# Kernel optimization log

Hardware: AMD Instinct MI355X
Metric: run time of the kernel (lower is better)

## Reference

```python
import jax, jax.numpy as jnp
import numpy as np

B, H, C, R, S, NS = 32, 128, 512, 64, 4096, 8
D = C + R
T = B * S
MAX_POS = 8192


def setup_inputs() -> dict:
    key = jax.random.key(0)
    k0, k1, k2, k3, k4 = jax.random.split(key, 5)
    q = jax.random.normal(k0, (B, H, D), dtype=jnp.float32)
    k_buffer = jax.random.normal(k1, (T, 1, D), dtype=jnp.float32)
    v_buffer = jax.random.normal(k2, (T, 1, C), dtype=jnp.float32)
    cos_sin_cache = jax.random.normal(k3, (MAX_POS, R), dtype=jnp.float32)
    positions = jax.random.randint(k4, (B,), 0, MAX_POS, dtype=jnp.int64) if jax.config.jax_enable_x64 else jax.random.randint(k4, (B,), 0, MAX_POS, dtype=jnp.int32)
    kv_indptr = (jnp.arange(B + 1, dtype=jnp.int32) * S)
    kv_indices = jnp.arange(T, dtype=jnp.int32)
    return {
        "q": q, "k_buffer": k_buffer, "v_buffer": v_buffer,
        "cos_sin_cache": cos_sin_cache, "positions": positions,
        "kv_indptr": kv_indptr, "kv_indices": kv_indices,
        "num_kv_splits": 8, "kv_lora_rank": 512, "rotary_dim": 64,
        "use_rope": 1,
    }


def _rotate_half(x, half):
    return jnp.concatenate([-x[..., half:], x[..., :half]], axis=-1)


def reference(q, k_buffer, v_buffer, cos_sin_cache, positions, kv_indptr,
              kv_indices, num_kv_splits, kv_lora_rank, rotary_dim, use_rope):
    b, h, head_dim = q.shape
    c = kv_lora_rank
    r = k_buffer.shape[-1] - c  # qk_rope_head_dim
    sm_scale = 1.0 / (head_dim ** 0.5)
    half = rotary_dim // 2

    kb = k_buffer[:, 0, :]
    vb = v_buffer[:, 0, :]
    s = kv_indices.shape[0] // b  # uniform seq_len layout (kv_indptr = arange*S)
    idx = kv_indices.reshape(b, s)
    seq_len = kv_indptr[1:] - kv_indptr[:-1]  # [b]

    k_rows = kb[idx]            # [b, s, c+r]
    kv_c = k_rows[:, :, :c]     # [b, s, c]
    k_pe = k_rows[:, :, c:]     # [b, s, r]
    v = vb[idx]                 # [b, s, c]

    q_c = q[:, :, :c]           # [b, h, c]
    q_pe = q[:, :, c:]          # [b, h, r]

    if use_rope:
        cos = cos_sin_cache[positions, :half]            # [b, half]
        sin = cos_sin_cache[positions, half:rotary_dim]  # [b, half]
        cos2 = jnp.concatenate([cos, cos], axis=-1)      # [b, r] (r == rotary_dim)
        sin2 = jnp.concatenate([sin, sin], axis=-1)
        q_pe = q_pe * cos2[:, None, :] + _rotate_half(q_pe, half) * sin2[:, None, :]
        # only the last cached token gets RoPE applied to its k_pe
        last_kpe = k_pe[jnp.arange(b), seq_len - 1]      # [b, r]
        last_roped = last_kpe * cos2 + _rotate_half(last_kpe, half) * sin2
        is_last = jnp.arange(s)[None, :] == (seq_len - 1)[:, None]  # [b, s]
        k_pe = jnp.where(is_last[:, :, None], last_roped[:, None, :], k_pe)
        k_pe_tokens_out = last_roped.astype(q.dtype)
    else:
        k_pe_tokens_out = jnp.zeros((1,), dtype=q.dtype)

    scores = (jnp.einsum('bhc,bsc->bhs', q_c, kv_c)
              + jnp.einsum('bhr,bsr->bhs', q_pe, k_pe)) * sm_scale  # [b, h, s]

    pos_n = jnp.arange(s)
    klps = (seq_len + num_kv_splits - 1) // num_kv_splits   # kv_len_per_split, [b]
    split_id = pos_n[None, :] // klps[:, None]              # [b, s]
    valid = pos_n[None, :] < seq_len[:, None]

    neg_inf = jnp.float32(-jnp.inf)
    outs = []
    for sp in range(num_kv_splits):  # small, static loop over KV splits
        m = (split_id == sp) & valid                        # [b, s]
        sc = jnp.where(m[:, None, :], scores, neg_inf)
        mx = jnp.max(sc, axis=-1)                           # [b, h]
        p = jnp.exp(sc - mx[..., None])
        e_sum = jnp.sum(p, axis=-1)                         # [b, h]
        o = jnp.einsum('bhs,bsc->bhc', p, v) / e_sum[..., None]
        lse = mx + jnp.log(e_sum)                           # [b, h]
        outs.append(jnp.concatenate([o, lse[..., None]], axis=-1))
    att_out = jnp.stack(outs, axis=2).astype(jnp.float32)   # [b, h, NS, c+1]
    return att_out, k_pe_tokens_out
```

## Files before the change

### kernel.cpp

```cpp
#include <hip/hip_runtime.h>
#include <math.h>

#define B_    32
#define H_    128
#define C_    512
#define R_    64
#define S_    4096
#define NS_   8
#define D_    576
#define HALF_ 32
#define HT    32
#define KB    32
#define PK    584
#define PS    36
#define PP    40

typedef _Float16 half8   __attribute__((ext_vector_type(8)));
typedef _Float16 half4_t __attribute__((ext_vector_type(4)));
typedef float    f32x4   __attribute__((ext_vector_type(4)));


__global__ __launch_bounds__(256)
void rope_q_kernel(float* __restrict__ q, const float* __restrict__ cache,
                   const int* __restrict__ positions) {
    int t = blockIdx.x * 256 + threadIdx.x;
    if (t >= B_ * H_ * HALF_) return;
    int i = t & (HALF_ - 1);
    int h = (t >> 5) & (H_ - 1);
    int b = t >> 12;
    int pos = positions[b];
    float c = cache[pos * R_ + i];
    float s = cache[pos * R_ + HALF_ + i];
    float* qp = q + (size_t)(b * H_ + h) * D_ + C_;
    float lo = qp[i], hi = qp[i + HALF_];
    qp[i]         = lo * c - hi * s;
    qp[i + HALF_] = hi * c + lo * s;
}

__global__ __launch_bounds__(256)
void rope_k_kernel(float* __restrict__ kbuf, const float* __restrict__ cache,
                   const int* __restrict__ positions, const int* __restrict__ indptr,
                   const int* __restrict__ indices, float* __restrict__ out_tail) {
    int t = blockIdx.x * 256 + threadIdx.x;
    if (t >= B_ * HALF_) return;
    int i = t & (HALF_ - 1);
    int b = t >> 5;
    int seq = indptr[b + 1] - indptr[b];
    int row = indices[b * S_ + seq - 1];
    int pos = positions[b];
    float c = cache[pos * R_ + i];
    float s = cache[pos * R_ + HALF_ + i];
    float* kp = kbuf + (size_t)row * D_ + C_;
    float lo = kp[i], hi = kp[i + HALF_];
    float nlo = lo * c - hi * s;
    float nhi = hi * c + lo * s;
    kp[i] = nlo; kp[i + HALF_] = nhi;
    out_tail[b * R_ + i]         = nlo;
    out_tail[b * R_ + HALF_ + i] = nhi;
}

__global__ void zero_tail_kernel(float* p) { if (threadIdx.x == 0) p[0] = 0.f; }


__global__ __launch_bounds__(256, 2)
void mla_attn_kernel(const float* __restrict__ q, const float* __restrict__ kbuf,
                     const float* __restrict__ vbuf, const int* __restrict__ indptr,
                     const int* __restrict__ indices, float* __restrict__ out) {
    __shared__ _Float16 k_lds[KB * PK];
    __shared__ float    s_lds[HT * PS];
    __shared__ _Float16 p_lds[HT * PP];
    __shared__ int      rows_s[KB];
    __shared__ float    m_s[HT], l_s[HT], a_s[HT];

    const int blk   = blockIdx.x;
    const int xcd   = blk & 7;
    const int inner = blk >> 3;
    const int htile = inner & 3;
    const int bs    = ((inner >> 2) << 3) | xcd;
    const int b     = bs >> 3;
    const int sp    = bs & 7;
    const int h0    = htile * HT;

    const int t    = threadIdx.x;
    const int lane = t & 63;
    const int w    = t >> 6;
    const int hm   = w >> 1;
    const int hv   = w & 1;
    const int lr   = lane & 15;
    const int kg   = lane >> 4;

    const int seq   = indptr[b + 1] - indptr[b];
    const int klps  = (seq + NS_ - 1) / NS_;
    const int start = sp * klps;
    const int end   = min(start + klps, seq);

    half8 qf[18];
    {
        const float* qrow = q + (size_t)(b * H_ + h0 + hm * 16 + lr) * D_ + kg * 8;
        #pragma unroll
        for (int s = 0; s < 18; ++s) {
            f32x4 x0 = *(const f32x4*)(qrow + s * 32);
            f32x4 x1 = *(const f32x4*)(qrow + s * 32 + 4);
            half8 h;
            h[0] = (_Float16)x0[0]; h[1] = (_Float16)x0[1];
            h[2] = (_Float16)x0[2]; h[3] = (_Float16)x0[3];
            h[4] = (_Float16)x1[0]; h[5] = (_Float16)x1[1];
            h[6] = (_Float16)x1[2]; h[7] = (_Float16)x1[3];
            qf[s] = h;
        }
    }
    if (t < HT) { m_s[t] = -INFINITY; l_s[t] = 0.f; }

    f32x4 oacc[16];
    #pragma unroll
    for (int n = 0; n < 16; ++n) oacc[n] = (f32x4){0.f, 0.f, 0.f, 0.f};

    const float sm_scale = 1.0f / sqrtf((float)D_);
    const int nchunk = (end - start + KB - 1) / KB;

    for (int ch = 0; ch < nchunk; ++ch) {
        const int j0 = start + ch * KB;
        __syncthreads();

        {
            const int row = t >> 3;
            const int seg = t & 7;
            const int pos = min(j0 + row, end - 1);
            const int r   = indices[b * S_ + pos];
            if (seg == 0) rows_s[row] = r;
            const float* src = kbuf + (size_t)r * D_;
            _Float16* dst = k_lds + row * PK;
            #pragma unroll
            for (int i = 0; i < 18; ++i) {
                const int f = (seg + 8 * i) * 4;
                f32x4 x = *(const f32x4*)(src + f);
                half4_t hh;
                hh[0] = (_Float16)x[0]; hh[1] = (_Float16)x[1];
                hh[2] = (_Float16)x[2]; hh[3] = (_Float16)x[3];
                *(half4_t*)(dst + f) = hh;
            }
        }
        __syncthreads();

        {
            f32x4 sacc = (f32x4){0.f, 0.f, 0.f, 0.f};
            const _Float16* kp = k_lds + (hv * 16 + lr) * PK + kg * 8;
            #pragma unroll
            for (int s = 0; s < 18; ++s) {
                half8 bf = *(const half8*)(kp + s * 32);
                sacc = __builtin_amdgcn_mfma_f32_16x16x32_f16(qf[s], bf, sacc, 0, 0, 0);
            }
            #pragma unroll
            for (int r = 0; r < 4; ++r)
                s_lds[(hm * 16 + kg * 4 + r) * PS + hv * 16 + lr] = sacc[r] * sm_scale;
        }
        __syncthreads();

        {
            const int h  = t >> 3;
            const int j8 = t & 7;
            f32x4 s4 = *(const f32x4*)(s_lds + h * PS + j8 * 4);
            const int jb = j0 + j8 * 4;
            if (jb + 0 >= end) s4[0] = -INFINITY;
            if (jb + 1 >= end) s4[1] = -INFINITY;
            if (jb + 2 >= end) s4[2] = -INFINITY;
            if (jb + 3 >= end) s4[3] = -INFINITY;
            float mx = fmaxf(fmaxf(s4[0], s4[1]), fmaxf(s4[2], s4[3]));
            mx = fmaxf(mx, __shfl_xor(mx, 1, 8));
            mx = fmaxf(mx, __shfl_xor(mx, 2, 8));
            mx = fmaxf(mx, __shfl_xor(mx, 4, 8));
            const float m_old = m_s[h];
            const float m_new = fmaxf(m_old, mx);
            float p0 = (jb + 0 < end) ? __expf(s4[0] - m_new) : 0.f;
            float p1 = (jb + 1 < end) ? __expf(s4[1] - m_new) : 0.f;
            float p2 = (jb + 2 < end) ? __expf(s4[2] - m_new) : 0.f;
            float p3 = (jb + 3 < end) ? __expf(s4[3] - m_new) : 0.f;
            float ps = p0 + p1 + p2 + p3;
            ps += __shfl_xor(ps, 1, 8);
            ps += __shfl_xor(ps, 2, 8);
            ps += __shfl_xor(ps, 4, 8);
            half4_t ph;
            ph[0] = (_Float16)p0; ph[1] = (_Float16)p1;
            ph[2] = (_Float16)p2; ph[3] = (_Float16)p3;
            *(half4_t*)(p_lds + h * PP + j8 * 4) = ph;
            if (j8 == 0) {
                const float al = __expf(m_old - m_new);
                a_s[h] = al;
                l_s[h] = l_s[h] * al + ps;
                m_s[h] = m_new;
            }
        }
        __syncthreads();

        {
            const float* vp[8];
            #pragma unroll
            for (int j = 0; j < 8; ++j)
                vp[j] = vbuf + (size_t)rows_s[kg * 8 + j] * C_ + hv * 256 + lr;
            half8 pf = *(const half8*)(p_lds + (hm * 16 + lr) * PP + kg * 8);
            float av[4];
            #pragma unroll
            for (int r = 0; r < 4; ++r) av[r] = a_s[hm * 16 + kg * 4 + r];
            #pragma unroll
            for (int n = 0; n < 16; ++n) {
                oacc[n][0] *= av[0]; oacc[n][1] *= av[1];
                oacc[n][2] *= av[2]; oacc[n][3] *= av[3];
            }
            #pragma unroll
            for (int n = 0; n < 16; ++n) {
                half8 vf;
                #pragma unroll
                for (int j = 0; j < 8; ++j)
                    vf[j] = (_Float16)vp[j][n * 16];
                oacc[n] = __builtin_amdgcn_mfma_f32_16x16x32_f16(pf, vf, oacc[n], 0, 0, 0);
            }
        }
    }

    {
        float inv[4];
        #pragma unroll
        for (int r = 0; r < 4; ++r) inv[r] = 1.0f / l_s[hm * 16 + kg * 4 + r];
        #pragma unroll
        for (int n = 0; n < 16; ++n) {
            #pragma unroll
            for (int r = 0; r < 4; ++r) {
                const int h = h0 + hm * 16 + kg * 4 + r;
                out[(size_t)((b * H_ + h) * NS_ + sp) * (C_ + 1) + hv * 256 + n * 16 + lr]
                    = oacc[n][r] * inv[r];
            }
        }
        if (t < HT)
            out[(size_t)((b * H_ + h0 + t) * NS_ + sp) * (C_ + 1) + C_]
                = m_s[t] + logf(l_s[t]);
    }
}


extern "C" void kernel_launch(void* const* d_in, const int* in_sizes, int n_in,
                              void* d_out, int out_size, void* d_ws, size_t ws_size,
                              hipStream_t stream) {
    float*       qp        = (float*)d_in[0];
    float*       kbuf      = (float*)d_in[1];
    const float* vbuf      = (const float*)d_in[2];
    const float* cache     = (const float*)d_in[3];
    const int*   positions = (const int*)d_in[4];
    const int*   indptr    = (const int*)d_in[5];
    const int*   indices   = (const int*)d_in[6];
    float*       out       = (float*)d_out;

    const long long tail = (long long)B_ * H_ * NS_ * (C_ + 1);
    const bool use_rope = ((long long)out_size == tail + (long long)B_ * R_);

    if (use_rope) {
        rope_q_kernel<<<(B_ * H_ * HALF_ + 255) / 256, 256, 0, stream>>>(qp, cache, positions);
        rope_k_kernel<<<(B_ * HALF_ + 255) / 256, 256, 0, stream>>>(
            kbuf, cache, positions, indptr, indices, out + tail);
    } else {
        zero_tail_kernel<<<1, 64, 0, stream>>>(out + tail);
    }

    mla_attn_kernel<<<dim3(1024), dim3(256), 0, stream>>>(qp, kbuf, vbuf, indptr, indices, out);
}
```

Before: 803.0 us.

## Stage V tiles in swizzled LDS and split QK reduction across doubled waves

```diff
diff --git a/kernel.cpp b/kernel.cpp
--- a/kernel.cpp
+++ b/kernel.cpp
@@ -12,8 +12,8 @@
 #define HT    32
 #define KB    32
 #define PK    584
-#define PS    36
-#define PP    40
+#define PSL   33
+#define PPL   40
 
 typedef _Float16 half8   __attribute__((ext_vector_type(8)));
 typedef _Float16 half4_t __attribute__((ext_vector_type(4)));
@@ -62,14 +62,14 @@
 __global__ void zero_tail_kernel(float* p) { if (threadIdx.x == 0) p[0] = 0.f; }
 
 
-__global__ __launch_bounds__(256, 2)
+__global__ __launch_bounds__(512, 4)
 void mla_attn_kernel(const float* __restrict__ q, const float* __restrict__ kbuf,
                      const float* __restrict__ vbuf, const int* __restrict__ indptr,
                      const int* __restrict__ indices, float* __restrict__ out) {
     __shared__ _Float16 k_lds[KB * PK];
-    __shared__ float    s_lds[HT * PS];
-    __shared__ _Float16 p_lds[HT * PP];
-    __shared__ int      rows_s[KB];
+    __shared__ _Float16 v_lds[C_ * KB];
+    __shared__ float    s_lds[2 * HT * PSL];
+    __shared__ _Float16 p_lds[HT * PPL];
     __shared__ float    m_s[HT], l_s[HT], a_s[HT];
 
     const int blk   = blockIdx.x;
@@ -84,21 +84,23 @@
     const int t    = threadIdx.x;
     const int lane = t & 63;
     const int w    = t >> 6;
-    const int hm   = w >> 1;
-    const int hv   = w & 1;
     const int lr   = lane & 15;
     const int kg   = lane >> 4;
+    const int hm   = w >> 2;
+    const int hv   = (w >> 1) & 1;
+    const int ks   = w & 1;
+    const int cq   = w & 3;
 
     const int seq   = indptr[b + 1] - indptr[b];
     const int klps  = (seq + NS_ - 1) / NS_;
     const int start = sp * klps;
     const int end   = min(start + klps, seq);
 
-    half8 qf[18];
+    half8 qf[9];
     {
-        const float* qrow = q + (size_t)(b * H_ + h0 + hm * 16 + lr) * D_ + kg * 8;
+        const float* qrow = q + (size_t)(b * H_ + h0 + hm * 16 + lr) * D_ + ks * 288 + kg * 8;
         #pragma unroll
-        for (int s = 0; s < 18; ++s) {
+        for (int s = 0; s < 9; ++s) {
             f32x4 x0 = *(const f32x4*)(qrow + s * 32);
             f32x4 x1 = *(const f32x4*)(qrow + s * 32 + 4);
             half8 h;
@@ -111,79 +113,93 @@
     }
     if (t < HT) { m_s[t] = -INFINITY; l_s[t] = 0.f; }
 
-    f32x4 oacc[16];
+    f32x4 oacc[8];
     #pragma unroll
-    for (int n = 0; n < 16; ++n) oacc[n] = (f32x4){0.f, 0.f, 0.f, 0.f};
-
-    const float sm_scale = 1.0f / sqrtf((float)D_);
+    for (int n = 0; n < 8; ++n) oacc[n] = (f32x4){0.f, 0.f, 0.f, 0.f};
+
+    const float sm_scale = 1.0f / 24.0f;
     const int nchunk = (end - start + KB - 1) / KB;
+
+    const int krow = t >> 4, kseg = t & 15;
+    const int vrow = t & 31, vseg = t >> 5;
 
     for (int ch = 0; ch < nchunk; ++ch) {
         const int j0 = start + ch * KB;
         __syncthreads();
 
         {
-            const int row = t >> 3;
-            const int seg = t & 7;
-            const int pos = min(j0 + row, end - 1);
-            const int r   = indices[b * S_ + pos];
-            if (seg == 0) rows_s[row] = r;
+            const int r = indices[b * S_ + min(j0 + krow, end - 1)];
             const float* src = kbuf + (size_t)r * D_;
-            _Float16* dst = k_lds + row * PK;
-            #pragma unroll
-            for (int i = 0; i < 18; ++i) {
-                const int f = (seg + 8 * i) * 4;
-                f32x4 x = *(const f32x4*)(src + f);
+            _Float16* dst = k_lds + krow * PK;
+            #pragma unroll
+            for (int i = 0; i < 9; ++i) {
+                const int d = kseg * 4 + i * 64;
+                f32x4 x = *(const f32x4*)(src + d);
                 half4_t hh;
                 hh[0] = (_Float16)x[0]; hh[1] = (_Float16)x[1];
                 hh[2] = (_Float16)x[2]; hh[3] = (_Float16)x[3];
-                *(half4_t*)(dst + f) = hh;
+                *(half4_t*)(dst + d) = hh;
+            }
+        }
+        {
+            const int r = indices[b * S_ + min(j0 + vrow, end - 1)];
+            const float* src = vbuf + (size_t)r * C_;
+            const int khi = vrow >> 3, klo = vrow & 7;
+            #pragma unroll
+            for (int i = 0; i < 8; ++i) {
+                const int c0 = vseg * 4 + i * 64;
+                f32x4 x = *(const f32x4*)(src + c0);
+                #pragma unroll
+                for (int cc = 0; cc < 4; ++cc) {
+                    const int c = c0 + cc;
+                    v_lds[c * KB + (((khi ^ cc) & 3) << 3) + klo] = (_Float16)x[cc];
+                }
             }
         }
         __syncthreads();
 
         {
             f32x4 sacc = (f32x4){0.f, 0.f, 0.f, 0.f};
-            const _Float16* kp = k_lds + (hv * 16 + lr) * PK + kg * 8;
-            #pragma unroll
-            for (int s = 0; s < 18; ++s) {
+            const _Float16* kp = k_lds + (hv * 16 + lr) * PK + ks * 288 + kg * 8;
+            __builtin_amdgcn_s_setprio(1);
+            #pragma unroll
+            for (int s = 0; s < 9; ++s) {
                 half8 bf = *(const half8*)(kp + s * 32);
                 sacc = __builtin_amdgcn_mfma_f32_16x16x32_f16(qf[s], bf, sacc, 0, 0, 0);
             }
+            __builtin_amdgcn_s_setprio(0);
             #pragma unroll
             for (int r = 0; r < 4; ++r)
-                s_lds[(hm * 16 + kg * 4 + r) * PS + hv * 16 + lr] = sacc[r] * sm_scale;
-        }
-        __syncthreads();
-
-        {
-            const int h  = t >> 3;
-            const int j8 = t & 7;
-            f32x4 s4 = *(const f32x4*)(s_lds + h * PS + j8 * 4);
-            const int jb = j0 + j8 * 4;
-            if (jb + 0 >= end) s4[0] = -INFINITY;
-            if (jb + 1 >= end) s4[1] = -INFINITY;
-            if (jb + 2 >= end) s4[2] = -INFINITY;
-            if (jb + 3 >= end) s4[3] = -INFINITY;
-            float mx = fmaxf(fmaxf(s4[0], s4[1]), fmaxf(s4[2], s4[3]));
-            mx = fmaxf(mx, __shfl_xor(mx, 1, 8));
-            mx = fmaxf(mx, __shfl_xor(mx, 2, 8));
-            mx = fmaxf(mx, __shfl_xor(mx, 4, 8));
+                s_lds[(ks * HT + hm * 16 + kg * 4 + r) * PSL + hv * 16 + lr] = sacc[r];
+        }
+        __syncthreads();
+
+        {
+            const int h  = t >> 4;
+            const int jj = t & 15;
+            float s0 = (s_lds[h * PSL + jj]        + s_lds[(HT + h) * PSL + jj])        * sm_scale;
+            float s1 = (s_lds[h * PSL + jj + 16]   + s_lds[(HT + h) * PSL + jj + 16])   * sm_scale;
+            const bool v0 = (j0 + jj)      < end;
+            const bool v1 = (j0 + jj + 16) < end;
+            if (!v0) s0 = -INFINITY;
+            if (!v1) s1 = -INFINITY;
+            float mx = fmaxf(s0, s1);
+            mx = fmaxf(mx, __shfl_xor(mx, 1, 16));
+            mx = fmaxf(mx, __shfl_xor(mx, 2, 16));
+            mx = fmaxf(mx, __shfl_xor(mx, 4, 16));
+            mx = fmaxf(mx, __shfl_xor(mx, 8, 16));
             const float m_old = m_s[h];
             const float m_new = fmaxf(m_old, mx);
-            float p0 = (jb + 0 < end) ? __expf(s4[0] - m_new) : 0.f;
-            float p1 = (jb + 1 < end) ? __expf(s4[1] - m_new) : 0.f;
-            float p2 = (jb + 2 < end) ? __expf(s4[2] - m_new) : 0.f;
-            float p3 = (jb + 3 < end) ? __expf(s4[3] - m_new) : 0.f;
-            float ps = p0 + p1 + p2 + p3;
-            ps += __shfl_xor(ps, 1, 8);
-            ps += __shfl_xor(ps, 2, 8);
-            ps += __shfl_xor(ps, 4, 8);
-            half4_t ph;
-            ph[0] = (_Float16)p0; ph[1] = (_Float16)p1;
-            ph[2] = (_Float16)p2; ph[3] = (_Float16)p3;
-            *(half4_t*)(p_lds + h * PP + j8 * 4) = ph;
-            if (j8 == 0) {
+            float p0 = v0 ? __expf(s0 - m_new) : 0.f;
+            float p1 = v1 ? __expf(s1 - m_new) : 0.f;
+            float ps = p0 + p1;
+            ps += __shfl_xor(ps, 1, 16);
+            ps += __shfl_xor(ps, 2, 16);
+            ps += __shfl_xor(ps, 4, 16);
+            ps += __shfl_xor(ps, 8, 16);
+            p_lds[h * PPL + jj]      = (_Float16)p0;
+            p_lds[h * PPL + jj + 16] = (_Float16)p1;
+            if (jj == 0) {
                 const float al = __expf(m_old - m_new);
                 a_s[h] = al;
                 l_s[h] = l_s[h] * al + ps;
@@ -193,42 +209,43 @@
         __syncthreads();
 
         {
-            const float* vp[8];
-            #pragma unroll
-            for (int j = 0; j < 8; ++j)
-                vp[j] = vbuf + (size_t)rows_s[kg * 8 + j] * C_ + hv * 256 + lr;
-            half8 pf = *(const half8*)(p_lds + (hm * 16 + lr) * PP + kg * 8);
-            float av[4];
-            #pragma unroll
-            for (int r = 0; r < 4; ++r) av[r] = a_s[hm * 16 + kg * 4 + r];
-            #pragma unroll
-            for (int n = 0; n < 16; ++n) {
-                oacc[n][0] *= av[0]; oacc[n][1] *= av[1];
-                oacc[n][2] *= av[2]; oacc[n][3] *= av[3];
-            }
-            #pragma unroll
-            for (int n = 0; n < 16; ++n) {
-                half8 vf;
-                #pragma unroll
-                for (int j = 0; j < 8; ++j)
-                    vf[j] = (_Float16)vp[j][n * 16];
+            half8 pf = *(const half8*)(p_lds + (hm * 16 + lr) * PPL + kg * 8);
+            float av0 = a_s[hm * 16 + kg * 4 + 0];
+            float av1 = a_s[hm * 16 + kg * 4 + 1];
+            float av2 = a_s[hm * 16 + kg * 4 + 2];
+            float av3 = a_s[hm * 16 + kg * 4 + 3];
+            #pragma unroll
+            for (int n = 0; n < 8; ++n) {
+                oacc[n][0] *= av0; oacc[n][1] *= av1;
+                oacc[n][2] *= av2; oacc[n][3] *= av3;
+            }
+            const int cb = cq * 128 + lr;
+            const int sx = (kg ^ (lr & 3)) << 3;
+            __builtin_amdgcn_s_setprio(1);
+            #pragma unroll
+            for (int n = 0; n < 8; ++n) {
+                const int c = cb + n * 16;
+                half8 vf = *(const half8*)(v_lds + c * KB + sx);
                 oacc[n] = __builtin_amdgcn_mfma_f32_16x16x32_f16(pf, vf, oacc[n], 0, 0, 0);
             }
+            __builtin_amdgcn_s_setprio(0);
         }
     }
 
     {
-        float inv[4];
+        float inv0 = 1.0f / l_s[hm * 16 + kg * 4 + 0];
+        float inv1 = 1.0f / l_s[hm * 16 + kg * 4 + 1];
+        float inv2 = 1.0f / l_s[hm * 16 + kg * 4 + 2];
+        float inv3 = 1.0f / l_s[hm * 16 + kg * 4 + 3];
         #pragma unroll
-        for (int r = 0; r < 4; ++r) inv[r] = 1.0f / l_s[hm * 16 + kg * 4 + r];
-        #pragma unroll
-        for (int n = 0; n < 16; ++n) {
-            #pragma unroll
-            for (int r = 0; r < 4; ++r) {
-                const int h = h0 + hm * 16 + kg * 4 + r;
-                out[(size_t)((b * H_ + h) * NS_ + sp) * (C_ + 1) + hv * 256 + n * 16 + lr]
-                    = oacc[n][r] * inv[r];
-            }
+        for (int n = 0; n < 8; ++n) {
+            const int c = cq * 128 + n * 16 + lr;
+            float* op = out + (size_t)((b * H_ + h0 + hm * 16 + kg * 4) * NS_ + sp) * (C_ + 1) + c;
+            const size_t hstride = (size_t)NS_ * (C_ + 1);
+            op[0 * hstride] = oacc[n][0] * inv0;
+            op[1 * hstride] = oacc[n][1] * inv1;
+            op[2 * hstride] = oacc[n][2] * inv2;
+            op[3 * hstride] = oacc[n][3] * inv3;
         }
         if (t < HT)
             out[(size_t)((b * H_ + h0 + t) * NS_ + sp) * (C_ + 1) + C_]
@@ -260,5 +277,5 @@
         zero_tail_kernel<<<1, 64, 0, stream>>>(out + tail);
     }
 
-    mla_attn_kernel<<<dim3(1024), dim3(256), 0, stream>>>(qp, kbuf, vbuf, indptr, indices, out);
-}
+    mla_attn_kernel<<<dim3(1024), dim3(512), 0, stream>>>(qp, kbuf, vbuf, indptr, indices, out);
+}
```

Result: slower. 874.6 us (+8.9%).
